# Kernel optimization log

Hardware: AMD Instinct MI355X
Metric: run time of the kernel (lower is better)

Reference implementation:

```python
import jax, jax.numpy as jnp
import numpy as np

B, T, D_IN, D_OUT, N_HEAD = 2, 2048, 1024, 1024, 16
HEAD_DIM = D_OUT // N_HEAD


def setup_inputs() -> dict:
    key = jax.random.key(0)
    k1, k2, k3, k4 = jax.random.split(key, 4)
    s = 0.02  # init scale for weights
    return {
        "x": jax.random.normal(k1, (B, T, D_IN), jnp.float32),
        "Wq": jax.random.normal(k2, (D_OUT, D_IN), jnp.float32) * s,
        "Wk": jax.random.normal(k3, (D_OUT, D_IN), jnp.float32) * s,
        "Wv": jax.random.normal(k4, (D_OUT, D_IN), jnp.float32) * s,
    }


def reference(x, Wq, Wk, Wv):
    b, t, _ = x.shape
    h, hd = N_HEAD, HEAD_DIM
    # Linear projections (torch Linear: x @ W.T), split heads -> [b,h,t,hd]
    q = (x @ Wq.T).reshape(b, t, h, hd).transpose(0, 2, 1, 3)
    k = (x @ Wk.T).reshape(b, t, h, hd).transpose(0, 2, 1, 3)
    v = (x @ Wv.T).reshape(b, t, h, hd).transpose(0, 2, 1, 3)
    # raw scores [b,h,t,t], causal mask BEFORE scaling (as in source)
    omega = jnp.einsum("bhqd,bhkd->bhqk", q, k)
    causal = jnp.triu(jnp.ones((t, t), dtype=bool), k=1)
    omega = jnp.where(causal, -jnp.inf, omega)
    attw = jax.nn.softmax(omega / jnp.sqrt(jnp.asarray(hd, omega.dtype)), axis=-1)
    ctx = jnp.einsum("bhqk,bhkd->bhqd", attw, v)  # [b,h,t,hd]
    # Faithful to source: transpose(2,3) then view(B,T,d_out)
    out = jnp.swapaxes(ctx, 2, 3).reshape(b, t, D_OUT)
    return out
```

## Files before the change

### kernel.cpp

```cpp
#include <hip/hip_runtime.h>
#include <hip/hip_bf16.h>
#include <stdint.h>

typedef __attribute__((ext_vector_type(8))) short s16x8;
typedef __attribute__((ext_vector_type(4))) float f32x4;

#define T_   2048
#define NH   16
#define HD   64
#define DIN  1024
#define SCALE_LOG2 0.18033688011112042f

#define MFMA32(a, b, c) __builtin_amdgcn_mfma_f32_16x16x32_bf16(a, b, c, 0, 0, 0)

__device__ __forceinline__ unsigned short f2bf(float f) {
  union { float f; uint32_t u; } c; c.f = f;
  uint32_t u = c.u;
  return (unsigned short)((u + 0x7FFFu + ((u >> 16) & 1u)) >> 16);
}

__device__ __forceinline__ uint32_t pk_bf16(float a, float b) {
  __hip_bfloat162 h = __float22bfloat162_rn(make_float2(a, b));
  return *reinterpret_cast<uint32_t*>(&h);
}

#define GLL(gp, lp) __builtin_amdgcn_global_load_lds( \
    (__attribute__((address_space(1))) void*)(gp),    \
    (__attribute__((address_space(3))) void*)(lp), 16, 0, 0)

__global__ __launch_bounds__(256) void cvt_kernel(
    const float* __restrict__ x,  const float* __restrict__ wq,
    const float* __restrict__ wk, const float* __restrict__ wv,
    unsigned short* __restrict__ xb, unsigned short* __restrict__ wb) {
  int i = (blockIdx.x * 256 + threadIdx.x) * 4;
  float4 v;
  unsigned short* dp;
  if (i < 4194304) {
    v = *(const float4*)(x + i);
    dp = xb + i;
  } else {
    int j = i - 4194304;
    int seg = j >> 20, r = j & 1048575;
    const float* w = (seg == 0) ? wq : (seg == 1) ? wk : wv;
    v = *(const float4*)(w + r);
    dp = wb + j;
  }
  ushort4 o;
  o.x = f2bf(v.x); o.y = f2bf(v.y); o.z = f2bf(v.z); o.w = f2bf(v.w);
  *(ushort4*)dp = o;
}

__global__ __launch_bounds__(256) void qkv_gemm(
    const unsigned short* __restrict__ A, const unsigned short* __restrict__ Bm,
    unsigned short* __restrict__ qkv) {
  __shared__ __attribute__((aligned(16))) unsigned short Alds[64 * 64];
  __shared__ __attribute__((aligned(16))) unsigned short Blds[128 * 64];
  const int tid = threadIdx.x;
  const int lane = tid & 63, wave = tid >> 6;
  const int wm = wave >> 1, wn = wave & 1;
  const int m0 = blockIdx.y * 64, n0 = blockIdx.x * 128;

  f32x4 acc[2][4] = {};

  const int srA = wave * 16 + (lane >> 3);
  const int srB = wave * 32 + (lane >> 3);
  const int scol = (((lane & 7) ^ ((lane >> 3) & 7))) * 8;
  const unsigned short* ag = A  + (size_t)(m0 + srA) * DIN + scol;
  const unsigned short* bg = Bm + (size_t)(n0 + srB) * DIN + scol;
  unsigned short* al = &Alds[wave * 16 * 64];
  unsigned short* bl = &Blds[wave * 32 * 64];

  const int l16 = lane & 15, quad = lane >> 4;
  const int sw = l16 & 7;

  for (int k0 = 0; k0 < DIN; k0 += 64) {
    __syncthreads();
#pragma unroll
    for (int i = 0; i < 2; i++)
      GLL(ag + (size_t)i * 8 * DIN + k0, al + i * 512);
#pragma unroll
    for (int i = 0; i < 4; i++)
      GLL(bg + (size_t)i * 8 * DIN + k0, bl + i * 512);
    __syncthreads();
#pragma unroll
    for (int ks = 0; ks < 2; ks++) {
      const int cl = ((ks * 4 + quad) ^ sw) * 8;
      s16x8 af[2], bf[4];
#pragma unroll
      for (int mt = 0; mt < 2; mt++)
        af[mt] = *(const s16x8*)&Alds[(wm * 32 + mt * 16 + l16) * 64 + cl];
#pragma unroll
      for (int nt = 0; nt < 4; nt++)
        bf[nt] = *(const s16x8*)&Blds[(wn * 64 + nt * 16 + l16) * 64 + cl];
#pragma unroll
      for (int mt = 0; mt < 2; mt++)
#pragma unroll
        for (int nt = 0; nt < 4; nt++)
          acc[mt][nt] = MFMA32(af[mt], bf[nt], acc[mt][nt]);
    }
  }

#pragma unroll
  for (int mt = 0; mt < 2; mt++) {
    int mbase = m0 + wm * 32 + mt * 16 + (quad << 2);
    int b = mbase >> 11, t = mbase & 2047;
#pragma unroll
    for (int nt = 0; nt < 4; nt++) {
      int n = n0 + wn * 64 + nt * 16 + l16;
      int sel = n >> 10, h = (n >> 6) & 15, d = n & 63;
      int bh = b * NH + h;
      if (sel == 2) {
        ushort4 pk;
        pk.x = f2bf(acc[mt][nt][0]); pk.y = f2bf(acc[mt][nt][1]);
        pk.z = f2bf(acc[mt][nt][2]); pk.w = f2bf(acc[mt][nt][3]);
        *(ushort4*)&qkv[8388608 + (size_t)(bh * HD + d) * T_ + t] = pk;
      } else {
        float qs = (sel == 0) ? SCALE_LOG2 : 1.f;
#pragma unroll
        for (int r = 0; r < 4; r++)
          qkv[(size_t)sel * 4194304 + (size_t)(bh * T_ + t + r) * HD + d] =
              f2bf(acc[mt][nt][r] * qs);
      }
    }
  }
}

__device__ __forceinline__ void tile_step(
    const unsigned short* Klds, const unsigned short* Vt,
    unsigned short* Plds, const s16x8 qf0, const s16x8 qf1,
    f32x4 o[4], f32x4& lacc,
    const int l16, const int quad, const int swl, const int wave,
    const bool diag) {
  f32x4 s[4] = {};
#pragma unroll
  for (int kk = 0; kk < 2; kk++) {
    const int cl = ((kk * 4 + quad) ^ swl) * 8;
    const s16x8 q = kk ? qf1 : qf0;
#pragma unroll
    for (int mt = 0; mt < 4; mt++) {
      s16x8 kf = *(const s16x8*)&Klds[(mt * 16 + l16) * 64 + cl];
      s[mt] = MFMA32(kf, q, s[mt]);
    }
  }

  uint32_t* prow = (uint32_t*)&Plds[(wave * 16 + l16) * 64];
  if (!diag) {
#pragma unroll
    for (int mt = 0; mt < 4; mt++) {
      float p0 = exp2f(s[mt][0]);
      float p1 = exp2f(s[mt][1]);
      float p2 = exp2f(s[mt][2]);
      float p3 = exp2f(s[mt][3]);
      *(uint2*)&prow[(((2 * mt + (quad >> 1)) ^ swl) << 2) + (quad & 1) * 2] =
          make_uint2(pk_bf16(p0, p1), pk_bf16(p2, p3));
    }
  } else {
    const int lim = wave * 16 + l16;
#pragma unroll
    for (int mt = 0; mt < 4; mt++) {
      const int kb = mt * 16 + quad * 4;
      float p0 = (kb + 0 <= lim) ? exp2f(s[mt][0]) : 0.f;
      float p1 = (kb + 1 <= lim) ? exp2f(s[mt][1]) : 0.f;
      float p2 = (kb + 2 <= lim) ? exp2f(s[mt][2]) : 0.f;
      float p3 = (kb + 3 <= lim) ? exp2f(s[mt][3]) : 0.f;
      *(uint2*)&prow[(((2 * mt + (quad >> 1)) ^ swl) << 2) + (quad & 1) * 2] =
          make_uint2(pk_bf16(p0, p1), pk_bf16(p2, p3));
    }
  }

  const s16x8 onesf = {0x3F80, 0x3F80, 0x3F80, 0x3F80,
                       0x3F80, 0x3F80, 0x3F80, 0x3F80};
  const unsigned short* prd = &Plds[(wave * 16 + l16) * 64];
#pragma unroll
  for (int kk = 0; kk < 2; kk++) {
    const int cl = ((kk * 4 + quad) ^ swl) * 8;
    s16x8 pf = *(const s16x8*)&prd[cl];
    lacc = MFMA32(pf, onesf, lacc);
#pragma unroll
    for (int dt = 0; dt < 4; dt++) {
      s16x8 vf = *(const s16x8*)&Vt[(dt * 16 + l16) * 64 + cl];
      o[dt] = MFMA32(pf, vf, o[dt]);
    }
  }
}

__global__ __launch_bounds__(256) void attn_kernel(
    const unsigned short* __restrict__ qkv, float* __restrict__ out) {
  __shared__ __attribute__((aligned(16))) unsigned short Klds[64 * 64];
  __shared__ __attribute__((aligned(16))) unsigned short Vt[64 * 64];
  __shared__ __attribute__((aligned(16))) unsigned short Plds[64 * 64];

  const int tid = threadIdx.x;
  const int lane = tid & 63, wave = tid >> 6;
  const int l16 = lane & 15, quad = lane >> 4;
  const int swl = l16 & 7;
  const int bh = blockIdx.x;
  const int qb = blockIdx.y;
  const int qa = 31 - qb;
  const size_t bh_off = (size_t)bh * (T_ * HD);
  const unsigned short* Q  = qkv + bh_off;
  const unsigned short* Kb = qkv + 4194304 + bh_off;
  const unsigned short* Vb = qkv + 8388608 + bh_off;

  s16x8 qfa0, qfa1, qfb0, qfb1;
  {
    const unsigned short* qp =
        Q + (size_t)(qa * 64 + wave * 16 + l16) * HD + quad * 8;
    qfa0 = *(const s16x8*)(qp);
    qfa1 = *(const s16x8*)(qp + 32);
    const unsigned short* qq =
        Q + (size_t)(qb * 64 + wave * 16 + l16) * HD + quad * 8;
    qfb0 = *(const s16x8*)(qq);
    qfb1 = *(const s16x8*)(qq + 32);
  }

  const int sr = tid >> 3;
  const int sc = (tid & 7) * 8;
  const int swc = (((tid & 7) ^ (sr & 7))) * 8;

  s16x8 kr0 = *(const s16x8*)&Kb[(size_t)sr * HD + sc];
  s16x8 kr1 = *(const s16x8*)&Kb[(size_t)(sr + 32) * HD + sc];
  s16x8 vr0 = *(const s16x8*)&Vb[(size_t)sr * T_ + sc];
  s16x8 vr1 = *(const s16x8*)&Vb[(size_t)(sr + 32) * T_ + sc];

  f32x4 oa[4] = {}, ob[4] = {};
  f32x4 la = {}, lb = {};

  for (int it = 0; it < 33; it++) {
    const bool pa = (it <= qa);
    __syncthreads();
    *(s16x8*)&Klds[sr * 64 + swc] = kr0;
    *(s16x8*)&Klds[(sr + 32) * 64 + swc] = kr1;
    *(s16x8*)&Vt[sr * 64 + swc] = vr0;
    *(s16x8*)&Vt[(sr + 32) * 64 + swc] = vr1;
    if (it < 32) {
      const int nk = (it < qa) ? it + 1 : it - qa;
      const unsigned short* kp = Kb + (size_t)nk * 64 * HD;
      const unsigned short* vp = Vb + nk * 64;
      kr0 = *(const s16x8*)&kp[(size_t)sr * HD + sc];
      kr1 = *(const s16x8*)&kp[(size_t)(sr + 32) * HD + sc];
      vr0 = *(const s16x8*)&vp[(size_t)sr * T_ + sc];
      vr1 = *(const s16x8*)&vp[(size_t)(sr + 32) * T_ + sc];
    }
    __syncthreads();

    if (pa)
      tile_step(Klds, Vt, Plds, qfa0, qfa1, oa, la, l16, quad, swl, wave,
                it == qa);
    else
      tile_step(Klds, Vt, Plds, qfb0, qfb1, ob, lb, l16, quad, swl, wave,
                it == 32);
  }

#pragma unroll
  for (int half = 0; half < 2; half++) {
    const f32x4* o = half ? ob : oa;
    const f32x4 lacc = half ? lb : la;
    const int q0 = (half ? qb : qa) * 64;
    f32x4 inv;
#pragma unroll
    for (int r = 0; r < 4; r++) inv[r] = 1.f / lacc[r];
#pragma unroll
    for (int dt = 0; dt < 4; dt++) {
      float4 v = make_float4(o[dt][0] * inv[0], o[dt][1] * inv[1],
                             o[dt][2] * inv[2], o[dt][3] * inv[3]);
      *(float4*)(out + (size_t)bh * (HD * T_) + (size_t)(dt * 16 + l16) * T_ +
                 q0 + wave * 16 + quad * 4) = v;
    }
  }
}

extern "C" void kernel_launch(void* const* d_in, const int* in_sizes, int n_in,
                              void* d_out, int out_size, void* d_ws, size_t ws_size,
                              hipStream_t stream) {
  const float* x  = (const float*)d_in[0];
  const float* wq = (const float*)d_in[1];
  const float* wk = (const float*)d_in[2];
  const float* wv = (const float*)d_in[3];
  float* out = (float*)d_out;

  unsigned short* xb  = (unsigned short*)d_ws;
  unsigned short* wb  = xb + 4194304;
  unsigned short* qkv = wb + 3145728;

  cvt_kernel<<<7168, 256, 0, stream>>>(x, wq, wk, wv, xb, wb);
  dim3 g1(24, 64);
  qkv_gemm<<<g1, 256, 0, stream>>>(xb, wb, qkv);
  dim3 g2(32, 16);
  attn_kernel<<<g2, 256, 0, stream>>>(qkv, out);
}
```

Baseline: 154.2 us.

## Double-buffer K/V tiles with direct global-to-LDS loads and a single barrier

Replaces the register-staged K/V prefetch (global load into registers, then an LDS store) with direct global-to-LDS loads (GLL) into a two-slot LDS buffer. The next tile streams into the alternate slot while the current one is processed. The XOR swizzle moves from the LDS write address to the global read column, since the direct loads write LDS contiguously. This removes the register round-trip and one __syncthreads per iteration. The trade-offs are double the K/V LDS footprint, which may lower occupancy, and a dependence on GLL waiting for its loads to finish before the barrier.

```diff
diff --git a/kernel.cpp b/kernel.cpp
--- a/kernel.cpp
+++ b/kernel.cpp
@@ -186,8 +186,8 @@
 
 __global__ __launch_bounds__(256) void attn_kernel(
     const unsigned short* __restrict__ qkv, float* __restrict__ out) {
-  __shared__ __attribute__((aligned(16))) unsigned short Klds[64 * 64];
-  __shared__ __attribute__((aligned(16))) unsigned short Vt[64 * 64];
+  __shared__ __attribute__((aligned(16))) unsigned short Kl[2][64 * 64];
+  __shared__ __attribute__((aligned(16))) unsigned short Vl[2][64 * 64];
   __shared__ __attribute__((aligned(16))) unsigned short Plds[64 * 64];
 
   const int tid = threadIdx.x;
@@ -214,42 +214,44 @@
     qfb1 = *(const s16x8*)(qq + 32);
   }
 
-  const int sr = tid >> 3;
-  const int sc = (tid & 7) * 8;
-  const int swc = (((tid & 7) ^ (sr & 7))) * 8;
-
-  s16x8 kr0 = *(const s16x8*)&Kb[(size_t)sr * HD + sc];
-  s16x8 kr1 = *(const s16x8*)&Kb[(size_t)(sr + 32) * HD + sc];
-  s16x8 vr0 = *(const s16x8*)&Vb[(size_t)sr * T_ + sc];
-  s16x8 vr1 = *(const s16x8*)&Vb[(size_t)(sr + 32) * T_ + sc];
+  const int r8 = lane >> 3;
+  const int xc = ((lane & 7) ^ r8) * 8;
+  const unsigned short* kg = Kb + (size_t)(wave * 16 + r8) * HD + xc;
+  const unsigned short* vg = Vb + (size_t)(wave * 16 + r8) * T_ + xc;
+  const int sbase = wave * 16 * 64;
 
   f32x4 oa[4] = {}, ob[4] = {};
   f32x4 la = {}, lb = {};
 
+#pragma unroll
+  for (int i = 0; i < 2; i++) {
+    GLL(kg + (size_t)i * 8 * HD, &Kl[0][sbase + i * 8 * 64]);
+    GLL(vg + (size_t)i * 8 * T_, &Vl[0][sbase + i * 8 * 64]);
+  }
+
+  int cur = 0;
   for (int it = 0; it < 33; it++) {
-    const bool pa = (it <= qa);
     __syncthreads();
-    *(s16x8*)&Klds[sr * 64 + swc] = kr0;
-    *(s16x8*)&Klds[(sr + 32) * 64 + swc] = kr1;
-    *(s16x8*)&Vt[sr * 64 + swc] = vr0;
-    *(s16x8*)&Vt[(sr + 32) * 64 + swc] = vr1;
     if (it < 32) {
       const int nk = (it < qa) ? it + 1 : it - qa;
-      const unsigned short* kp = Kb + (size_t)nk * 64 * HD;
-      const unsigned short* vp = Vb + nk * 64;
-      kr0 = *(const s16x8*)&kp[(size_t)sr * HD + sc];
-      kr1 = *(const s16x8*)&kp[(size_t)(sr + 32) * HD + sc];
-      vr0 = *(const s16x8*)&vp[(size_t)sr * T_ + sc];
-      vr1 = *(const s16x8*)&vp[(size_t)(sr + 32) * T_ + sc];
-    }
-    __syncthreads();
-
-    if (pa)
-      tile_step(Klds, Vt, Plds, qfa0, qfa1, oa, la, l16, quad, swl, wave,
-                it == qa);
+      const unsigned short* kp = kg + (size_t)nk * 64 * HD;
+      const unsigned short* vp = vg + nk * 64;
+      unsigned short* kd = &Kl[cur ^ 1][sbase];
+      unsigned short* vd = &Vl[cur ^ 1][sbase];
+#pragma unroll
+      for (int i = 0; i < 2; i++) {
+        GLL(kp + (size_t)i * 8 * HD, kd + i * 8 * 64);
+        GLL(vp + (size_t)i * 8 * T_, vd + i * 8 * 64);
+      }
+    }
+
+    if (it <= qa)
+      tile_step(Kl[cur], Vl[cur], Plds, qfa0, qfa1, oa, la, l16, quad, swl,
+                wave, it == qa);
     else
-      tile_step(Klds, Vt, Plds, qfb0, qfb1, ob, lb, l16, quad, swl, wave,
-                it == 32);
+      tile_step(Kl[cur], Vl[cur], Plds, qfb0, qfb1, ob, lb, l16, quad, swl,
+                wave, it == 32);
+    cur ^= 1;
   }
 
 #pragma unroll
```

New measurement: 157.4 us. +2.1%, slower.

## Split long causal query tiles across two blocks and combine partial results

Applied to the files above, without the earlier changes.

Replaces the paired-tile scheme, where each block handled two query tiles over 33 key steps, with 48 blocks per head. Each block handles one query tile, and query tiles 16-31 are split into two key ranges. Partial numerators and denominators for the split tiles go to workspace, and a new combine kernel sums them and normalizes. The aim is more blocks for better occupancy and load balance across CUs. The cost is an extra kernel launch, extra global traffic for partials, and a combine that relies on the softmax using no running max.

```diff
diff --git a/kernel.cpp b/kernel.cpp
--- a/kernel.cpp
+++ b/kernel.cpp
@@ -185,7 +185,8 @@
 }
 
 __global__ __launch_bounds__(256) void attn_kernel(
-    const unsigned short* __restrict__ qkv, float* __restrict__ out) {
+    const unsigned short* __restrict__ qkv, float* __restrict__ out,
+    float* __restrict__ op, float* __restrict__ lp) {
   __shared__ __attribute__((aligned(16))) unsigned short Klds[64 * 64];
   __shared__ __attribute__((aligned(16))) unsigned short Vt[64 * 64];
   __shared__ __attribute__((aligned(16))) unsigned short Plds[64 * 64];
@@ -195,48 +196,55 @@
   const int l16 = lane & 15, quad = lane >> 4;
   const int swl = l16 & 7;
   const int bh = blockIdx.x;
-  const int qb = blockIdx.y;
-  const int qa = 31 - qb;
+
+  const int y = blockIdx.y;
+  int j;
+  if (y < 18) {
+    j = (y == 0) ? 15 : ((y == 17) ? 47 : 15 + y);
+  } else {
+    const int z = y - 18, L = 15 - (z >> 1);
+    j = (z & 1) ? (L - 1) : (L + 31);
+  }
+  int qt, kt0, kt1, hi;
+  bool split;
+  if (j < 16)      { qt = j;      kt0 = 0;  kt1 = j;  split = false; hi = 0; }
+  else if (j < 32) { qt = j;      kt0 = 0;  kt1 = 15; split = true;  hi = 0; }
+  else             { qt = j - 16; kt0 = 16; kt1 = qt; split = true;  hi = 1; }
+
   const size_t bh_off = (size_t)bh * (T_ * HD);
   const unsigned short* Q  = qkv + bh_off;
   const unsigned short* Kb = qkv + 4194304 + bh_off;
   const unsigned short* Vb = qkv + 8388608 + bh_off;
 
-  s16x8 qfa0, qfa1, qfb0, qfb1;
+  s16x8 qf0, qf1;
   {
     const unsigned short* qp =
-        Q + (size_t)(qa * 64 + wave * 16 + l16) * HD + quad * 8;
-    qfa0 = *(const s16x8*)(qp);
-    qfa1 = *(const s16x8*)(qp + 32);
-    const unsigned short* qq =
-        Q + (size_t)(qb * 64 + wave * 16 + l16) * HD + quad * 8;
-    qfb0 = *(const s16x8*)(qq);
-    qfb1 = *(const s16x8*)(qq + 32);
+        Q + (size_t)(qt * 64 + wave * 16 + l16) * HD + quad * 8;
+    qf0 = *(const s16x8*)(qp);
+    qf1 = *(const s16x8*)(qp + 32);
   }
 
   const int sr = tid >> 3;
   const int sc = (tid & 7) * 8;
   const int swc = (((tid & 7) ^ (sr & 7))) * 8;
 
-  s16x8 kr0 = *(const s16x8*)&Kb[(size_t)sr * HD + sc];
-  s16x8 kr1 = *(const s16x8*)&Kb[(size_t)(sr + 32) * HD + sc];
-  s16x8 vr0 = *(const s16x8*)&Vb[(size_t)sr * T_ + sc];
-  s16x8 vr1 = *(const s16x8*)&Vb[(size_t)(sr + 32) * T_ + sc];
-
-  f32x4 oa[4] = {}, ob[4] = {};
-  f32x4 la = {}, lb = {};
-
-  for (int it = 0; it < 33; it++) {
-    const bool pa = (it <= qa);
+  s16x8 kr0 = *(const s16x8*)&Kb[(size_t)(kt0 * 64 + sr) * HD + sc];
+  s16x8 kr1 = *(const s16x8*)&Kb[(size_t)(kt0 * 64 + sr + 32) * HD + sc];
+  s16x8 vr0 = *(const s16x8*)&Vb[(size_t)sr * T_ + kt0 * 64 + sc];
+  s16x8 vr1 = *(const s16x8*)&Vb[(size_t)(sr + 32) * T_ + kt0 * 64 + sc];
+
+  f32x4 o[4] = {};
+  f32x4 lacc = {};
+
+  for (int kt = kt0; kt <= kt1; kt++) {
     __syncthreads();
     *(s16x8*)&Klds[sr * 64 + swc] = kr0;
     *(s16x8*)&Klds[(sr + 32) * 64 + swc] = kr1;
     *(s16x8*)&Vt[sr * 64 + swc] = vr0;
     *(s16x8*)&Vt[(sr + 32) * 64 + swc] = vr1;
-    if (it < 32) {
-      const int nk = (it < qa) ? it + 1 : it - qa;
-      const unsigned short* kp = Kb + (size_t)nk * 64 * HD;
-      const unsigned short* vp = Vb + nk * 64;
+    if (kt < kt1) {
+      const unsigned short* kp = Kb + (size_t)(kt + 1) * 64 * HD;
+      const unsigned short* vp = Vb + (kt + 1) * 64;
       kr0 = *(const s16x8*)&kp[(size_t)sr * HD + sc];
       kr1 = *(const s16x8*)&kp[(size_t)(sr + 32) * HD + sc];
       vr0 = *(const s16x8*)&vp[(size_t)sr * T_ + sc];
@@ -244,19 +252,11 @@
     }
     __syncthreads();
 
-    if (pa)
-      tile_step(Klds, Vt, Plds, qfa0, qfa1, oa, la, l16, quad, swl, wave,
-                it == qa);
-    else
-      tile_step(Klds, Vt, Plds, qfb0, qfb1, ob, lb, l16, quad, swl, wave,
-                it == 32);
-  }
-
-#pragma unroll
-  for (int half = 0; half < 2; half++) {
-    const f32x4* o = half ? ob : oa;
-    const f32x4 lacc = half ? lb : la;
-    const int q0 = (half ? qb : qa) * 64;
+    tile_step(Klds, Vt, Plds, qf0, qf1, o, lacc, l16, quad, swl, wave,
+              kt == qt);
+  }
+
+  if (!split) {
     f32x4 inv;
 #pragma unroll
     for (int r = 0; r < 4; r++) inv[r] = 1.f / lacc[r];
@@ -265,8 +265,40 @@
       float4 v = make_float4(o[dt][0] * inv[0], o[dt][1] * inv[1],
                              o[dt][2] * inv[2], o[dt][3] * inv[3]);
       *(float4*)(out + (size_t)bh * (HD * T_) + (size_t)(dt * 16 + l16) * T_ +
-                 q0 + wave * 16 + quad * 4) = v;
-    }
+                 qt * 64 + wave * 16 + quad * 4) = v;
+    }
+  } else {
+    const int slot = ((bh * 16 + (qt - 16)) << 1) + hi;
+    float* Op = op + (size_t)slot * 4096;
+    float* Lp = lp + (size_t)slot * 64;
+#pragma unroll
+    for (int dt = 0; dt < 4; dt++) {
+      float4 v = make_float4(o[dt][0], o[dt][1], o[dt][2], o[dt][3]);
+      *(float4*)(Op + (dt * 16 + l16) * 64 + wave * 16 + quad * 4) = v;
+    }
+    if (l16 == 0) {
+#pragma unroll
+      for (int r = 0; r < 4; r++) Lp[wave * 16 + quad * 4 + r] = lacc[r];
+    }
+  }
+}
+
+__global__ __launch_bounds__(256) void combine_kernel(
+    const float* __restrict__ op, const float* __restrict__ lp,
+    float* __restrict__ out) {
+  const int bh = blockIdx.x, j2 = blockIdx.y;
+  const int slot = (bh * 16 + j2) << 1;
+  const float* Olo = op + (size_t)slot * 4096;
+  const float* Ohi = Olo + 4096;
+  const float* Llo = lp + (size_t)slot * 64;
+  const int t = threadIdx.x;
+  const int q = t & 63, d0 = (t >> 6) * 16;
+  const float inv = 1.f / (Llo[q] + Llo[64 + q]);
+  float* ob = out + (size_t)bh * (HD * T_) + (size_t)(j2 + 16) * 64 + q;
+#pragma unroll
+  for (int dd = 0; dd < 16; dd++) {
+    const int d = d0 + dd;
+    ob[(size_t)d * T_] = (Olo[d * 64 + q] + Ohi[d * 64 + q]) * inv;
   }
 }
 
@@ -282,10 +314,14 @@
   unsigned short* xb  = (unsigned short*)d_ws;
   unsigned short* wb  = xb + 4194304;
   unsigned short* qkv = wb + 3145728;
+  float* op = (float*)(qkv + 12582912);
+  float* lp = op + 4194304;
 
   cvt_kernel<<<7168, 256, 0, stream>>>(x, wq, wk, wv, xb, wb);
   dim3 g1(24, 64);
   qkv_gemm<<<g1, 256, 0, stream>>>(xb, wb, qkv);
-  dim3 g2(32, 16);
-  attn_kernel<<<g2, 256, 0, stream>>>(qkv, out);
-}
+  dim3 g2(32, 48);
+  attn_kernel<<<g2, 256, 0, stream>>>(qkv, out, op, lp);
+  dim3 g3(32, 16);
+  combine_kernel<<<g3, 256, 0, stream>>>(op, lp, out);
+}
```

Result: faster. 150.4 us (-2.4%).
